# Kernel optimization log

Hardware: AMD Instinct MI355X
Metric: run time of the kernel (lower is better)

Reference implementation:

```python
import jax, jax.numpy as jnp
import numpy as np

B, T, F, H = 64, 512, 1024, 1024

def setup_inputs() -> dict:
    key = jax.random.key(0)
    k1, k2, k3 = jax.random.split(key, 3)
    x = jax.random.normal(k1, (B, T, F), dtype=jnp.float32)
    # fused gate kernels, flax gate order: i, f, g, o
    Wx = jax.random.normal(k2, (F, 4 * H), dtype=jnp.float32) / np.sqrt(F).astype(np.float32)
    Wh = jax.random.normal(k3, (H, 4 * H), dtype=jnp.float32) / np.sqrt(H).astype(np.float32)
    b = jnp.zeros((4 * H,), dtype=jnp.float32)
    return {"x": x, "Wx": Wx, "Wh": Wh, "b": b}

def reference(x, Wx, Wh, b):
    """Unidirectional LSTM matching flax OptimizedLSTMCell scanned over axis 1.

    x: [B, T, F] -> hs: [B, T, H]
    """
    Bb = x.shape[0]
    Hh = Wh.shape[0]
    # Precompute the input projection for all timesteps (same math, one big GEMM).
    xg = jnp.einsum('btf,fg->btg', x, Wx)  # [B, T, 4H]

    def step(carry, xt):
        c, h = carry
        z = xt + h @ Wh + b                     # [B, 4H]
        i, f, g, o = jnp.split(z, 4, axis=-1)   # flax gate order i,f,g,o
        new_c = jax.nn.sigmoid(f) * c + jax.nn.sigmoid(i) * jnp.tanh(g)
        new_h = jax.nn.sigmoid(o) * jnp.tanh(new_c)
        return (new_c, new_h), new_h

    c0 = jnp.zeros((Bb, Hh), dtype=x.dtype)
    h0 = jnp.zeros((Bb, Hh), dtype=x.dtype)
    (_, _), hs = jax.lax.scan(step, (c0, h0), jnp.swapaxes(xg, 0, 1))  # time-major scan
    return jnp.swapaxes(hs, 0, 1)  # [B, T, H]
```

## Files before the change

### kernel.cpp

```cpp
#include <hip/hip_runtime.h>
#include <hip/hip_bf16.h>
#include <stdint.h>

typedef __bf16 bf16x8 __attribute__((ext_vector_type(8)));
typedef float  floatx4 __attribute__((ext_vector_type(4)));

static constexpr int kT = 512, kH = 1024, k4H = 4096;

__global__ void pack_w(const float* __restrict__ Wx, const float* __restrict__ Wh,
                       __bf16* __restrict__ wpk) {
  int idx = blockIdx.x * 256 + threadIdx.x;
  int l  = idx & 63;
  int c  = (idx >> 6) & 63;
  int np = idx >> 12;
  int nl = l & 15;
  int g  = nl & 3, hl = nl >> 2;
  int col = g * kH + np * 4 + hl;
  int kf  = (l >> 4) * 8;
  const float* src = (c < 32) ? Wx + (size_t)(c * 32 + kf) * k4H + col
                              : Wh + (size_t)((c - 32) * 32 + kf) * k4H + col;
  bf16x8 v;
#pragma unroll
  for (int j = 0; j < 8; ++j) v[j] = (__bf16)src[(size_t)j * k4H];
  *(bf16x8*)(wpk + (size_t)idx * 8) = v;
}

__global__ void pack_x(const float* __restrict__ x, __bf16* __restrict__ xpk) {
  int idx = blockIdx.x * 256 + threadIdx.x;
  int l  = idx & 63;
  int c  = (idx >> 6) & 31;
  int mt = (idx >> 11) & 3;
  int t  = idx >> 13;
  int m  = mt * 16 + (l & 15);
  int f  = c * 32 + (l >> 4) * 8;
  const float4* src = (const float4*)(x + ((size_t)m * kT + t) * 1024 + f);
  float4 r0 = src[0], r1 = src[1];
  bf16x8 v;
  v[0] = (__bf16)r0.x; v[1] = (__bf16)r0.y; v[2] = (__bf16)r0.z; v[3] = (__bf16)r0.w;
  v[4] = (__bf16)r1.x; v[5] = (__bf16)r1.y; v[6] = (__bf16)r1.z; v[7] = (__bf16)r1.w;
  *(bf16x8*)(xpk + (size_t)idx * 8) = v;
}

__launch_bounds__(512, 2)
__global__ void lstm_scan(const __bf16* __restrict__ xpk, const __bf16* __restrict__ wpk,
                          const float* __restrict__ bias, uint32_t* __restrict__ hd,
                          int* __restrict__ sent, float* __restrict__ out) {
  const int blk  = blockIdx.x;
  const int half = blk & 1;
  const int mq   = (blk >> 1) & 3;
  const int cg   = half * 32 + (blk >> 3);
  const int tid  = threadIdx.x;
  const int wave = tid >> 6;
  const int lane = tid & 63;

  __shared__ __align__(16) float zbuf[8][16][68];

  bf16x8 breg[4][8];
#pragma unroll
  for (int nt = 0; nt < 4; ++nt) {
    const __bf16* wsrc = wpk + (((size_t)(cg * 4 + nt) * 64 + wave * 8) * 64 + lane) * 8;
#pragma unroll
    for (int cc = 0; cc < 8; ++cc)
      breg[nt][cc] = *(const bf16x8*)(wsrc + (size_t)cc * 512);
  }
#pragma unroll
  for (int nt = 0; nt < 4; ++nt)
#pragma unroll
    for (int cc = 0; cc < 8; ++cc)
      asm volatile("" : "+v"(breg[nt][cc]));

  const int gm   = (tid >> 4) & 15;
  const int ghc  = tid & 15;
  const int m_g  = mq * 16 + gm;
  const int hcol = cg * 16 + ghc;
  const int gnt  = ghc >> 2, ghl = ghc & 3;
  float c_state  = 0.f;
  const float bi = bias[0 * kH + hcol], bf_ = bias[1 * kH + hcol];
  const float bg = bias[2 * kH + hcol], bo  = bias[3 * kH + hcol];
  const int hdoff = ((mq * 128 + cg * 2 + (ghc >> 3)) * 16 + gm) * 4 + ((ghc & 7) >> 1);

  floatx4 acc[4];
#pragma unroll
  for (int nt = 0; nt < 4; ++nt) acc[nt] = floatx4{0.f, 0.f, 0.f, 0.f};

  if (wave < 4) {
    const __bf16* asrc = xpk + ((size_t)mq * 32 + wave * 8) * 512 + (size_t)lane * 8;
#pragma unroll
    for (int cc = 0; cc < 8; ++cc) {
      bf16x8 a = *(const bf16x8*)(asrc + (size_t)cc * 512);
#pragma unroll
      for (int nt = 0; nt < 4; ++nt)
        acc[nt] = __builtin_amdgcn_mfma_f32_16x16x32_bf16(a, breg[nt][cc], acc[nt], 0, 0, 0);
    }
  }

#pragma unroll 1
  for (int t = 0; t < kT; ++t) {
#pragma unroll
    for (int nt = 0; nt < 4; ++nt)
#pragma unroll
      for (int rr = 0; rr < 4; ++rr)
        zbuf[wave][(lane >> 4) * 4 + rr][nt * 16 + (lane & 15)] = acc[nt][rr];
    __syncthreads();

    if (tid < 256) {
      float zi = bi, zf = bf_, zg = bg, zo = bo;
      const float* zp = &zbuf[0][gm][gnt * 16 + ghl * 4];
#pragma unroll
      for (int w = 0; w < 8; ++w) {
        floatx4 zv = *(const floatx4*)(zp + (size_t)w * 16 * 68);
        zi += zv[0]; zf += zv[1]; zg += zv[2]; zo += zv[3];
      }
      float ig = 1.f / (1.f + __expf(-zi));
      float fg = 1.f / (1.f + __expf(-zf));
      float gg = 2.f / (1.f + __expf(-2.f * zg)) - 1.f;
      float og = 1.f / (1.f + __expf(-zo));
      c_state = fg * c_state + ig * gg;
      float tc = 2.f / (1.f + __expf(-2.f * c_state)) - 1.f;
      float h  = og * tc;
      __bf16 hb16 = (__bf16)h;
      uint16_t hbits;
      __builtin_memcpy(&hbits, &hb16, 2);
      uint32_t mine = hbits;
      uint32_t partner = (uint32_t)__shfl_xor((int)mine, 1);
      if ((ghc & 1) == 0) {
        uint32_t packed = mine | (partner << 16);
        __hip_atomic_store(&hd[(size_t)(t & 3) * 32768 + hdoff], packed,
                           __ATOMIC_RELAXED, __HIP_MEMORY_SCOPE_AGENT);
      }
      __builtin_nontemporal_store(h, &out[((size_t)m_g * kT + t) * kH + hcol]);
    }
    __syncthreads();

    if (tid == 0)
      __hip_atomic_store(&sent[(((t & 7) * 4 + mq) * 4 + (cg >> 4)) * 16 + (cg & 15)], t,
                         __ATOMIC_RELAXED, __HIP_MEMORY_SCOPE_AGENT);

    if (t < kT - 1) {
#pragma unroll
      for (int nt = 0; nt < 4; ++nt) acc[nt] = floatx4{0.f, 0.f, 0.f, 0.f};
      if (wave < 4) {
        const __bf16* asrc = xpk + (((size_t)(t + 1) * 4 + mq) * 32 + wave * 8) * 512
                           + (size_t)lane * 8;
#pragma unroll
        for (int cc = 0; cc < 8; ++cc) {
          bf16x8 a = __builtin_nontemporal_load((const bf16x8*)(asrc + (size_t)cc * 512));
#pragma unroll
          for (int nt = 0; nt < 4; ++nt)
            acc[nt] = __builtin_amdgcn_mfma_f32_16x16x32_bf16(a, breg[nt][cc], acc[nt], 0, 0, 0);
        }
      } else {
        const int s = wave - 4;
        const int* sline = sent + (((t & 7) * 4 + mq) * 4 + s) * 16 + (lane & 15);
        int guard = 0;
        for (;;) {
          int v = __hip_atomic_load(sline, __ATOMIC_RELAXED, __HIP_MEMORY_SCOPE_AGENT);
          if (__all(v == t)) break;
          __builtin_amdgcn_s_sleep(2);
          if (++guard > (1 << 20)) break;
        }
        asm volatile("" ::: "memory");
        const uint64_t* hb = (const uint64_t*)hd + (size_t)(t & 3) * 16384
                           + ((size_t)(mq * 128 + s * 32 + (lane >> 4)) * 16 + (lane & 15)) * 2;
        uint64_t w[8][2];
#pragma unroll
        for (int c = 0; c < 8; ++c) {
          w[c][0] = __hip_atomic_load(hb + (size_t)c * 128,     __ATOMIC_RELAXED,
                                      __HIP_MEMORY_SCOPE_AGENT);
          w[c][1] = __hip_atomic_load(hb + (size_t)c * 128 + 1, __ATOMIC_RELAXED,
                                      __HIP_MEMORY_SCOPE_AGENT);
        }
#pragma unroll
        for (int c = 0; c < 8; ++c) {
          union { uint64_t q[2]; bf16x8 v; } u;
          u.q[0] = w[c][0]; u.q[1] = w[c][1];
#pragma unroll
          for (int nt = 0; nt < 4; ++nt)
            acc[nt] = __builtin_amdgcn_mfma_f32_16x16x32_bf16(u.v, breg[nt][c], acc[nt], 0, 0, 0);
        }
      }
    }
  }
}

extern "C" void kernel_launch(void* const* d_in, const int* in_sizes, int n_in,
                              void* d_out, int out_size, void* d_ws, size_t ws_size,
                              hipStream_t stream) {
  const float* x  = (const float*)d_in[0];
  const float* Wx = (const float*)d_in[1];
  const float* Wh = (const float*)d_in[2];
  const float* b  = (const float*)d_in[3];
  float* out = (float*)d_out;

  char* ws = (char*)d_ws;
  int*      snt = (int*)ws;
  uint32_t* hdb = (uint32_t*)(ws + ((size_t)1 << 16));
  __bf16*   wpk = (__bf16*)(ws + ((size_t)1 << 20));
  __bf16*   xpk = (__bf16*)(ws + ((size_t)17 << 20));
  (void)in_sizes; (void)n_in; (void)out_size; (void)ws_size;

  hipLaunchKernelGGL(pack_w, dim3(4096),  dim3(256), 0, stream, Wx, Wh, wpk);
  hipLaunchKernelGGL(pack_x, dim3(16384), dim3(256), 0, stream, x, xpk);
  hipLaunchKernelGGL(lstm_scan, dim3(256), dim3(512), 0, stream,
                     xpk, wpk, b, hdb, snt, out);
}
```

Before: 1.856 ms.

## Replace per-block sentinel flags with timestep-tagged hidden-state words

Each hidden-state word now carries the timestep in its upper 32 bits, so consumer waves poll the data itself instead of a separate sentinel array. This removes the second block barrier before the flag store and one serialized flag-then-data round trip per step. Consumers re-load only the words whose tag does not yet match. Barriers are replaced with raw s_barrier plus an explicit LDS waitcnt. The cost is that each h word is twice as wide (64-bit loads and stores), and a memset is needed to invalidate tags before launch.

```diff
diff --git a/kernel.cpp b/kernel.cpp
--- a/kernel.cpp
+++ b/kernel.cpp
@@ -43,8 +43,8 @@
 
 __launch_bounds__(512, 2)
 __global__ void lstm_scan(const __bf16* __restrict__ xpk, const __bf16* __restrict__ wpk,
-                          const float* __restrict__ bias, uint32_t* __restrict__ hd,
-                          int* __restrict__ sent, float* __restrict__ out) {
+                          const float* __restrict__ bias, uint64_t* __restrict__ hq,
+                          float* __restrict__ out) {
   const int blk  = blockIdx.x;
   const int half = blk & 1;
   const int mq   = (blk >> 1) & 3;
@@ -77,7 +77,7 @@
   float c_state  = 0.f;
   const float bi = bias[0 * kH + hcol], bf_ = bias[1 * kH + hcol];
   const float bg = bias[2 * kH + hcol], bo  = bias[3 * kH + hcol];
-  const int hdoff = ((mq * 128 + cg * 2 + (ghc >> 3)) * 16 + gm) * 4 + ((ghc & 7) >> 1);
+  const int qoff = ((mq * 512 + cg * 8 + (ghc >> 1)) * 16) + gm;
 
   floatx4 acc[4];
 #pragma unroll
@@ -101,7 +101,9 @@
 #pragma unroll
       for (int rr = 0; rr < 4; ++rr)
         zbuf[wave][(lane >> 4) * 4 + rr][nt * 16 + (lane & 15)] = acc[nt][rr];
-    __syncthreads();
+    asm volatile("s_waitcnt lgkmcnt(0)" ::: "memory");
+    __builtin_amdgcn_s_barrier();
+    asm volatile("" ::: "memory");
 
     if (tid < 256) {
       float zi = bi, zf = bf_, zg = bg, zo = bo;
@@ -124,17 +126,16 @@
       uint32_t mine = hbits;
       uint32_t partner = (uint32_t)__shfl_xor((int)mine, 1);
       if ((ghc & 1) == 0) {
-        uint32_t packed = mine | (partner << 16);
-        __hip_atomic_store(&hd[(size_t)(t & 3) * 32768 + hdoff], packed,
+        uint64_t qw = ((uint64_t)(uint32_t)t << 32)
+                    | (uint64_t)(mine | (partner << 16));
+        __hip_atomic_store(&hq[(size_t)(t & 3) * 32768 + qoff], qw,
                            __ATOMIC_RELAXED, __HIP_MEMORY_SCOPE_AGENT);
       }
       __builtin_nontemporal_store(h, &out[((size_t)m_g * kT + t) * kH + hcol]);
     }
-    __syncthreads();
-
-    if (tid == 0)
-      __hip_atomic_store(&sent[(((t & 7) * 4 + mq) * 4 + (cg >> 4)) * 16 + (cg & 15)], t,
-                         __ATOMIC_RELAXED, __HIP_MEMORY_SCOPE_AGENT);
+    asm volatile("" ::: "memory");
+    __builtin_amdgcn_s_barrier();
+    asm volatile("" ::: "memory");
 
     if (t < kT - 1) {
 #pragma unroll
@@ -151,29 +152,41 @@
         }
       } else {
         const int s = wave - 4;
-        const int* sline = sent + (((t & 7) * 4 + mq) * 4 + s) * 16 + (lane & 15);
+        const uint64_t* hb = hq + (size_t)(t & 3) * 32768 + (size_t)mq * 8192
+                           + (size_t)s * 2048 + (lane >> 4) * 64 + (lane & 15);
+        const uint32_t tagv = (uint32_t)t;
+        uint64_t w[8][4];
+#pragma unroll
+        for (int c = 0; c < 8; ++c)
+#pragma unroll
+          for (int d = 0; d < 4; ++d)
+            w[c][d] = __hip_atomic_load(hb + (size_t)c * 256 + d * 16,
+                                        __ATOMIC_RELAXED, __HIP_MEMORY_SCOPE_AGENT);
         int guard = 0;
         for (;;) {
-          int v = __hip_atomic_load(sline, __ATOMIC_RELAXED, __HIP_MEMORY_SCOPE_AGENT);
-          if (__all(v == t)) break;
+          bool ok = true;
+#pragma unroll
+          for (int c = 0; c < 8; ++c)
+#pragma unroll
+            for (int d = 0; d < 4; ++d)
+              ok = ok && ((uint32_t)(w[c][d] >> 32) == tagv);
+          if (__all(ok)) break;
           __builtin_amdgcn_s_sleep(2);
+#pragma unroll
+          for (int c = 0; c < 8; ++c)
+#pragma unroll
+            for (int d = 0; d < 4; ++d)
+              if ((uint32_t)(w[c][d] >> 32) != tagv)
+                w[c][d] = __hip_atomic_load(hb + (size_t)c * 256 + d * 16,
+                                            __ATOMIC_RELAXED, __HIP_MEMORY_SCOPE_AGENT);
           if (++guard > (1 << 20)) break;
         }
         asm volatile("" ::: "memory");
-        const uint64_t* hb = (const uint64_t*)hd + (size_t)(t & 3) * 16384
-                           + ((size_t)(mq * 128 + s * 32 + (lane >> 4)) * 16 + (lane & 15)) * 2;
-        uint64_t w[8][2];
 #pragma unroll
         for (int c = 0; c < 8; ++c) {
-          w[c][0] = __hip_atomic_load(hb + (size_t)c * 128,     __ATOMIC_RELAXED,
-                                      __HIP_MEMORY_SCOPE_AGENT);
-          w[c][1] = __hip_atomic_load(hb + (size_t)c * 128 + 1, __ATOMIC_RELAXED,
-                                      __HIP_MEMORY_SCOPE_AGENT);
-        }
-#pragma unroll
-        for (int c = 0; c < 8; ++c) {
-          union { uint64_t q[2]; bf16x8 v; } u;
-          u.q[0] = w[c][0]; u.q[1] = w[c][1];
+          union { uint32_t d[4]; bf16x8 v; } u;
+#pragma unroll
+          for (int d0 = 0; d0 < 4; ++d0) u.d[d0] = (uint32_t)w[c][d0];
 #pragma unroll
           for (int nt = 0; nt < 4; ++nt)
             acc[nt] = __builtin_amdgcn_mfma_f32_16x16x32_bf16(u.v, breg[nt][c], acc[nt], 0, 0, 0);
@@ -193,14 +206,15 @@
   float* out = (float*)d_out;
 
   char* ws = (char*)d_ws;
-  int*      snt = (int*)ws;
-  uint32_t* hdb = (uint32_t*)(ws + ((size_t)1 << 16));
+  uint64_t* hdq = (uint64_t*)ws;
   __bf16*   wpk = (__bf16*)(ws + ((size_t)1 << 20));
   __bf16*   xpk = (__bf16*)(ws + ((size_t)17 << 20));
   (void)in_sizes; (void)n_in; (void)out_size; (void)ws_size;
 
+  hipMemsetAsync(hdq, 0xFF, (size_t)1 << 20, stream);
+
   hipLaunchKernelGGL(pack_w, dim3(4096),  dim3(256), 0, stream, Wx, Wh, wpk);
   hipLaunchKernelGGL(pack_x, dim3(16384), dim3(256), 0, stream, x, xpk);
   hipLaunchKernelGGL(lstm_scan, dim3(256), dim3(512), 0, stream,
-                     xpk, wpk, b, hdb, snt, out);
-}
+                     xpk, wpk, b, hdq, out);
+}
```

Result: slower. 2.368 ms (+27.6%).
